# Kernel tuning notes

Measured on AMD Instinct MI355X. Metric: run time of the kernel, lower is better.

## Reference

```python
import jax, jax.numpy as jnp
import numpy as np

D = 1024
H = 16
DH = D // H
SCALE = 1.0 / float(np.sqrt(DH))
EPS = 1e-5


def layer_norm(x, g, b):
    mu = jnp.mean(x, axis=-1, keepdims=True)
    var = jnp.mean((x - mu) ** 2, axis=-1, keepdims=True)
    return (x - mu) * jax.lax.rsqrt(var + EPS) * g + b


def setup_inputs() -> dict:
    key = jax.random.key(0)
    ks = jax.random.split(key, 12)
    B, N = 2, 2048
    x = jax.random.normal(ks[0], (B, N, D), dtype=jnp.float32)
    # sparse 0/1 adjacency (tree-like density) plus self loops
    adj = (jax.random.uniform(ks[1], (B, N, N)) < 0.002).astype(jnp.float32)
    adj = jnp.maximum(adj, jnp.eye(N, dtype=jnp.float32)[None])
    attn_mask = jnp.zeros((B, N, N), dtype=jnp.float32)
    s = 0.02
    params = {
        "qkv_w": jax.random.normal(ks[2], (D, 3 * D)) * s,
        "qkv_b": jnp.zeros((3 * D,), jnp.float32),
        "out_w": jax.random.normal(ks[3], (D, D)) * s,
        "out_b": jnp.zeros((D,), jnp.float32),
        "ln1_g": jnp.ones((D,), jnp.float32),
        "ln1_b": jnp.zeros((D,), jnp.float32),
        "ln2_g": jnp.ones((D,), jnp.float32),
        "ln2_b": jnp.zeros((D,), jnp.float32),
        "ff1_w": jax.random.normal(ks[4], (D, 4 * D)) * s,
        "ff1_b": jnp.zeros((4 * D,), jnp.float32),
        "ff2_w": jax.random.normal(ks[5], (4 * D, D)) * s,
        "ff2_b": jnp.zeros((D,), jnp.float32),
        "struct_bias": jnp.zeros((1,), jnp.float32) + 0.1,
    }
    return {"x": x, "adjacency": adj, "attn_mask": attn_mask, **params}


def reference(x, adjacency, attn_mask, qkv_w, qkv_b, out_w, out_b,
              ln1_g, ln1_b, ln2_g, ln2_b, ff1_w, ff1_b, ff2_w, ff2_b,
              struct_bias):
    b, n, d = x.shape
    residual = x
    h = layer_norm(x, ln1_g, ln1_b)
    qkv = (h @ qkv_w + qkv_b).reshape(b, n, 3, H, DH)
    q = jnp.transpose(qkv[:, :, 0], (0, 2, 1, 3))  # [B,H,N,Dh]
    k = jnp.transpose(qkv[:, :, 1], (0, 2, 1, 3))
    v = jnp.transpose(qkv[:, :, 2], (0, 2, 1, 3))
    scores = jnp.einsum("bhqd,bhkd->bhqk", q, k) * SCALE
    scores = scores + struct_bias[0] * adjacency[:, None] + attn_mask[:, None]
    attn = jax.nn.softmax(scores, axis=-1)  # dropout is identity at eval
    out = jnp.einsum("bhqk,bhkd->bhqd", attn, v)
    out = jnp.transpose(out, (0, 2, 1, 3)).reshape(b, n, d)
    out = out @ out_w + out_b
    x1 = residual + out
    h2 = layer_norm(x1, ln2_g, ln2_b)
    ff = jax.nn.gelu(h2 @ ff1_w + ff1_b, approximate=False) @ ff2_w + ff2_b
    return x1 + ff
```

## Files before the change

kernel.cpp:

```cpp
#include <hip/hip_runtime.h>
#include <math.h>

#define Dm 1024
#define Hh 16
#define DHh 64
#define Bb 2
#define Nn 2048
#define Rr 4096
#define SCALE_ 0.125f
#define EPS_ 1e-5f
#define SMAX_ 4.0f
#define LOG2E_ 1.4426950408889634f

typedef unsigned short u16;
typedef __attribute__((ext_vector_type(8))) short short8;
typedef __attribute__((ext_vector_type(4))) float f32x4;

__device__ __forceinline__ u16 f2bf(float f) {
  union { float f; unsigned u; } v; v.f = f;
  unsigned r = v.u + 0x7fffu + ((v.u >> 16) & 1u);
  return (u16)(r >> 16);
}
__device__ __forceinline__ float bf2f(u16 h) {
  union { unsigned u; float f; } v; v.u = ((unsigned)h) << 16;
  return v.f;
}
__device__ __forceinline__ unsigned pk2(float a, float b) {
  union { float f; unsigned u; } x, y; x.f = a; y.f = b;
  return (x.u >> 16) | (y.u & 0xffff0000u);
}

__device__ __forceinline__ void g2l16(const u16* g, const u16* l) {
  __builtin_amdgcn_global_load_lds(
      (const __attribute__((address_space(1))) void*)g,
      (__attribute__((address_space(3))) void*)l, 16, 0, 0);
}

__global__ void transpose_all(const float* __restrict__ qkv_w, const float* __restrict__ out_w,
                              const float* __restrict__ ff1_w, const float* __restrict__ ff2_w,
                              u16* __restrict__ qkvT, u16* __restrict__ outT,
                              u16* __restrict__ ff1T, u16* __restrict__ ff2T) {
  __shared__ float tile[32][33];
  int flat = blockIdx.x;
  const float* W; u16* WT; int K, N, local;
  if (flat < 3072)        { W = qkv_w; WT = qkvT; K = 1024; N = 3072; local = flat; }
  else if (flat < 4096)   { W = out_w; WT = outT; K = 1024; N = 1024; local = flat - 3072; }
  else if (flat < 8192)   { W = ff1_w; WT = ff1T; K = 1024; N = 4096; local = flat - 4096; }
  else                    { W = ff2_w; WT = ff2T; K = 4096; N = 1024; local = flat - 8192; }
  int nx = N / 32;
  int n0 = (local % nx) * 32, k0 = (local / nx) * 32;
  int tx = threadIdx.x, ty = threadIdx.y;
#pragma unroll
  for (int i = 0; i < 4; i++)
    tile[ty + 8 * i][tx] = W[(size_t)(k0 + ty + 8 * i) * N + n0 + tx];
  __syncthreads();
#pragma unroll
  for (int i = 0; i < 4; i++)
    WT[(size_t)(n0 + ty + 8 * i) * K + k0 + tx] = f2bf(tile[tx][ty + 8 * i]);
}

__global__ void bias_precompute(const float* __restrict__ adj, const float* __restrict__ mask,
                                const float* __restrict__ sbp, u16* __restrict__ bias16) {
  const float sb = sbp[0];
  const float C3 = -SMAX_ * LOG2E_;
  size_t i = ((size_t)blockIdx.x * 256 + threadIdx.x) * 8;
  float4 a0 = *(const float4*)(adj + i);
  float4 a1 = *(const float4*)(adj + i + 4);
  float4 m0 = *(const float4*)(mask + i);
  float4 m1 = *(const float4*)(mask + i + 4);
  ushort4 o0, o1;
  o0.x = f2bf(fmaf(fmaf(sb, a0.x, m0.x), LOG2E_, C3));
  o0.y = f2bf(fmaf(fmaf(sb, a0.y, m0.y), LOG2E_, C3));
  o0.z = f2bf(fmaf(fmaf(sb, a0.z, m0.z), LOG2E_, C3));
  o0.w = f2bf(fmaf(fmaf(sb, a0.w, m0.w), LOG2E_, C3));
  o1.x = f2bf(fmaf(fmaf(sb, a1.x, m1.x), LOG2E_, C3));
  o1.y = f2bf(fmaf(fmaf(sb, a1.y, m1.y), LOG2E_, C3));
  o1.z = f2bf(fmaf(fmaf(sb, a1.z, m1.z), LOG2E_, C3));
  o1.w = f2bf(fmaf(fmaf(sb, a1.w, m1.w), LOG2E_, C3));
  *(ushort4*)(bias16 + i) = o0;
  *(ushort4*)(bias16 + i + 4) = o1;
}

template <int BI>
__global__ void ln_kernel(const void* __restrict__ xin, const float* __restrict__ g,
                          const float* __restrict__ be, u16* __restrict__ out) {
  int row = blockIdx.x;
  int t = threadIdx.x;
  float4 v;
  if (BI) {
    ushort4 uv = ((const ushort4*)((const u16*)xin + (size_t)row * Dm))[t];
    v.x = bf2f(uv.x); v.y = bf2f(uv.y); v.z = bf2f(uv.z); v.w = bf2f(uv.w);
  } else {
    v = ((const float4*)((const float*)xin + (size_t)row * Dm))[t];
  }
  float s = v.x + v.y + v.z + v.w;
  float s2 = v.x * v.x + v.y * v.y + v.z * v.z + v.w * v.w;
#pragma unroll
  for (int o = 32; o > 0; o >>= 1) { s += __shfl_down(s, o); s2 += __shfl_down(s2, o); }
  __shared__ float sm[8];
  int w = t >> 6;
  if ((t & 63) == 0) { sm[w] = s; sm[4 + w] = s2; }
  __syncthreads();
  if (t == 0) {
    float a = sm[0] + sm[1] + sm[2] + sm[3];
    float a2 = sm[4] + sm[5] + sm[6] + sm[7];
    float mu = a * (1.f / Dm);
    sm[0] = mu;
    sm[1] = rsqrtf(a2 * (1.f / Dm) - mu * mu + EPS_);
  }
  __syncthreads();
  float mu = sm[0], rstd = sm[1];
  float4 gv = ((const float4*)g)[t];
  float4 bv = ((const float4*)be)[t];
  ushort4 o4;
  o4.x = f2bf((v.x - mu) * rstd * gv.x + bv.x);
  o4.y = f2bf((v.y - mu) * rstd * gv.y + bv.y);
  o4.z = f2bf((v.z - mu) * rstd * gv.z + bv.z);
  o4.w = f2bf((v.w - mu) * rstd * gv.w + bv.w);
  ((ushort4*)(out + (size_t)row * Dm))[t] = o4;
}

template <int MODE, int MI, int NI>
__global__ __launch_bounds__(256) void gemm_bt(
    const u16* __restrict__ A, const u16* __restrict__ BT,
    const float* __restrict__ bias, const void* __restrict__ res,
    void* __restrict__ Cout, u16* __restrict__ qb,
    u16* __restrict__ kb, u16* __restrict__ vb, int Ndim, int Kdim) {
  constexpr int TM = MI * 32, TN = NI * 32;
  constexpr int NS = (TM + TN) / 16;
  __shared__ u16 As[2][TM * 32];
  __shared__ u16 Bs[2][TN * 32];
  const int t = threadIdx.x;
  const int wave = t >> 6, lane = t & 63;
  const int wm = wave >> 1, wn = wave & 1;
  const int lr = lane & 15, lq = lane >> 4;
  const int flat = blockIdx.x + gridDim.x * blockIdx.y;
  constexpr int nMb = 4096 / TM;
  constexpr int mpx = nMb / 8;
  const int xcd = flat & 7;
  const int p = flat >> 3;
  const int m0 = (xcd * mpx + (p % mpx)) * TM;
  const int n0 = (p / mpx) * TN;

  auto stage = [&](int kt, int bsel) {
#pragma unroll
    for (int s = wave; s < NS; s += 4) {
      if (s < TM / 16)
        g2l16(A + (size_t)(m0 + s * 16 + (lane >> 2)) * Kdim + kt + (lane & 3) * 8,
              &As[bsel][(s * 16) * 32]);
      else
        g2l16(BT + (size_t)(n0 + (s - TM / 16) * 16 + (lane >> 2)) * Kdim + kt + (lane & 3) * 8,
              &Bs[bsel][((s - TM / 16) * 16) * 32]);
    }
  };

  f32x4 acc[MI][NI];
#pragma unroll
  for (int i = 0; i < MI; i++)
#pragma unroll
    for (int j = 0; j < NI; j++) acc[i][j] = (f32x4){0.f, 0.f, 0.f, 0.f};

  stage(0, 0);
  int cur = 0;
  for (int kt = 0; kt < Kdim; kt += 32) {
    __syncthreads();
    if (kt + 32 < Kdim) stage(kt + 32, cur ^ 1);
    short8 af[MI], bf[NI];
#pragma unroll
    for (int i = 0; i < MI; i++)
      af[i] = *(const short8*)&As[cur][(wm * (MI * 16) + i * 16 + lr) * 32 + lq * 8];
#pragma unroll
    for (int j = 0; j < NI; j++)
      bf[j] = *(const short8*)&Bs[cur][(wn * (NI * 16) + j * 16 + lr) * 32 + lq * 8];
#pragma unroll
    for (int i = 0; i < MI; i++)
#pragma unroll
      for (int j = 0; j < NI; j++)
        acc[i][j] = __builtin_amdgcn_mfma_f32_16x16x32_bf16(af[i], bf[j], acc[i][j], 0, 0, 0);
    cur ^= 1;
  }

#pragma unroll
  for (int i = 0; i < MI; i++) {
#pragma unroll
    for (int j = 0; j < NI; j++) {
#pragma unroll
      for (int r = 0; r < 4; r++) {
        int row = m0 + wm * (MI * 16) + i * 16 + lq * 4 + r;
        int col = n0 + wn * (NI * 16) + j * 16 + lr;
        float val = acc[i][j][r] + bias[col];
        if (MODE == 0) {
          int s = col >> 10, rem = col & 1023;
          int hh = rem >> 6, dh = rem & 63;
          int bi = row >> 11, ni = row & 2047;
          if (s == 2) {
            vb[(((size_t)bi * Hh + hh) * DHh + dh) * Nn + ni] = f2bf(val);
          } else {
            u16* dst = (s == 0) ? qb : kb;
            dst[(((size_t)bi * Hh + hh) * Nn + ni) * DHh + dh] = f2bf(val);
          }
        } else if (MODE == 1) {
          size_t o = (size_t)row * Ndim + col;
          ((u16*)Cout)[o] = f2bf(val + ((const float*)res)[o]);
        } else if (MODE == 3) {
          size_t o = (size_t)row * Ndim + col;
          ((float*)Cout)[o] = val + bf2f(((const u16*)res)[o]);
        } else {
          float u = val;
          float y2 = 1.5957691216f * fmaf(0.044715f * u, u * u, u);
          float gv = u / (1.f + __expf(-y2));
          size_t o = (size_t)row * Ndim + col;
          ((u16*)Cout)[o] = f2bf(gv);
        }
      }
    }
  }
}

__global__ __launch_bounds__(256) void attn_kernel(
    const u16* __restrict__ q, const u16* __restrict__ k, const u16* __restrict__ vT,
    const u16* __restrict__ bias16, u16* __restrict__ pO0, u16* __restrict__ pO1,
    float* __restrict__ pl) {
  const int qt = blockIdx.x, hb = blockIdx.y, kp = blockIdx.z;
  const int hh = hb & 15, b = hb >> 4;
  const int t = threadIdx.x, wave = t >> 6, lane = t & 63;
  const int lr = lane & 15, lq = lane >> 4;
  const size_t head_off = (((size_t)b * Hh + hh) * Nn) * DHh;
  const u16* Q = q + head_off;
  const u16* K = k + head_off;
  const u16* Vt = vT + head_off;
  const int q0 = qt * 128;
  const int kbase = kp * (Nn / 2);
  u16* pO = kp ? pO1 : pO0;

  __shared__ u16 Ks[64 * 72];
  __shared__ u16 VsT[64 * 72];
  __shared__ u16 Ps[4][32 * 72];

  short8 qf[2][2];
#pragma unroll
  for (int qs = 0; qs < 2; qs++) {
    const u16* Qr = Q + (size_t)(q0 + wave * 32 + qs * 16 + lr) * DHh;
    qf[qs][0] = *(const short8*)(Qr + lq * 8);
    qf[qs][1] = *(const short8*)(Qr + 32 + lq * 8);
  }
  f32x4 o_acc[2][4];
  float l_acc[2];
#pragma unroll
  for (int qs = 0; qs < 2; qs++) {
#pragma unroll
    for (int j = 0; j < 4; j++) o_acc[qs][j] = (f32x4){0.f, 0.f, 0.f, 0.f};
    l_acc[qs] = 0.f;
  }

  const int srow = t >> 2;
  const int sc0 = (t & 3) * 16;
  const int ssw = ((srow >> 2) & 3) << 4;
  const int wc0 = sc0 ^ ssw, wc1 = (sc0 + 8) ^ ssw;
  const u16* Kst = K + (size_t)srow * DHh + sc0;
  const u16* Vst = Vt + (size_t)srow * Nn + sc0;
  const int rsw = ((lr >> 2) & 3) << 4;

  const u16* bp = bias16 + ((size_t)b * Nn + q0 + wave * 32 + lr) * Nn;

  f32x4 kr0 = *(const f32x4*)(Kst + (size_t)kbase * DHh);
  f32x4 kr1 = *(const f32x4*)(Kst + (size_t)kbase * DHh + 8);
  f32x4 vr0 = *(const f32x4*)(Vst + kbase);
  f32x4 vr1 = *(const f32x4*)(Vst + kbase + 8);
  ushort4 bw[2][4];
#pragma unroll
  for (int qs = 0; qs < 2; qs++)
#pragma unroll
    for (int ns = 0; ns < 4; ns++)
      bw[qs][ns] = *(const ushort4*)(bp + (size_t)qs * 16 * Nn + kbase + ns * 16 + lq * 4);

  const float C1 = SCALE_ * LOG2E_;
  const int kend = kbase + Nn / 2;

  for (int kt = kbase; kt < kend; kt += 64) {
    __syncthreads();
    *(f32x4*)&Ks[srow * 72 + wc0] = kr0;
    *(f32x4*)&Ks[srow * 72 + wc1] = kr1;
    *(f32x4*)&VsT[srow * 72 + wc0] = vr0;
    *(f32x4*)&VsT[srow * 72 + wc1] = vr1;
    __syncthreads();
    if (kt + 64 < kend) {
      kr0 = *(const f32x4*)(Kst + (size_t)(kt + 64) * DHh);
      kr1 = *(const f32x4*)(Kst + (size_t)(kt + 64) * DHh + 8);
      vr0 = *(const f32x4*)(Vst + kt + 64);
      vr1 = *(const f32x4*)(Vst + kt + 64 + 8);
    }
    short8 kf[4][2];
#pragma unroll
    for (int ns = 0; ns < 4; ns++) {
      int row = ns * 16 + lr;
      kf[ns][0] = *(const short8*)&Ks[row * 72 + ((lq * 8) ^ rsw)];
      kf[ns][1] = *(const short8*)&Ks[row * 72 + ((32 + lq * 8) ^ rsw)];
    }
    f32x4 s0[4], s1[4];
#pragma unroll
    for (int ns = 0; ns < 4; ns++) {
      f32x4 z = (f32x4){0.f, 0.f, 0.f, 0.f};
      s0[ns] = __builtin_amdgcn_mfma_f32_16x16x32_bf16(kf[ns][0], qf[0][0], z, 0, 0, 0);
      s0[ns] = __builtin_amdgcn_mfma_f32_16x16x32_bf16(kf[ns][1], qf[0][1], s0[ns], 0, 0, 0);
      s1[ns] = __builtin_amdgcn_mfma_f32_16x16x32_bf16(kf[ns][0], qf[1][0], z, 0, 0, 0);
      s1[ns] = __builtin_amdgcn_mfma_f32_16x16x32_bf16(kf[ns][1], qf[1][1], s1[ns], 0, 0, 0);
    }
    float p0[4][4], p1[4][4];
#pragma unroll
    for (int ns = 0; ns < 4; ns++) {
      p0[ns][0] = exp2f(fmaf(s0[ns][0], C1, bf2f(bw[0][ns].x)));
      p0[ns][1] = exp2f(fmaf(s0[ns][1], C1, bf2f(bw[0][ns].y)));
      p0[ns][2] = exp2f(fmaf(s0[ns][2], C1, bf2f(bw[0][ns].z)));
      p0[ns][3] = exp2f(fmaf(s0[ns][3], C1, bf2f(bw[0][ns].w)));
      p1[ns][0] = exp2f(fmaf(s1[ns][0], C1, bf2f(bw[1][ns].x)));
      p1[ns][1] = exp2f(fmaf(s1[ns][1], C1, bf2f(bw[1][ns].y)));
      p1[ns][2] = exp2f(fmaf(s1[ns][2], C1, bf2f(bw[1][ns].z)));
      p1[ns][3] = exp2f(fmaf(s1[ns][3], C1, bf2f(bw[1][ns].w)));
      l_acc[0] += (p0[ns][0] + p0[ns][1]) + (p0[ns][2] + p0[ns][3]);
      l_acc[1] += (p1[ns][0] + p1[ns][1]) + (p1[ns][2] + p1[ns][3]);
    }
    if (kt + 64 < kend) {
#pragma unroll
      for (int qs = 0; qs < 2; qs++)
#pragma unroll
        for (int ns = 0; ns < 4; ns++)
          bw[qs][ns] = *(const ushort4*)(bp + (size_t)qs * 16 * Nn + kt + 64 + ns * 16 + lq * 4);
    }
#pragma unroll
    for (int ns = 0; ns < 4; ns++) {
      int sc = ((ns ^ ((lr >> 2) & 3)) << 4) + lq * 4;
      uint2 w0, w1;
      w0.x = pk2(p0[ns][0], p0[ns][1]); w0.y = pk2(p0[ns][2], p0[ns][3]);
      w1.x = pk2(p1[ns][0], p1[ns][1]); w1.y = pk2(p1[ns][2], p1[ns][3]);
      *(uint2*)&Ps[wave][lr * 72 + sc] = w0;
      *(uint2*)&Ps[wave][(16 + lr) * 72 + sc] = w1;
    }
    short8 pf[2][2];
#pragma unroll
    for (int qs = 0; qs < 2; qs++) {
      pf[qs][0] = *(const short8*)&Ps[wave][(qs * 16 + lr) * 72 + ((lq * 8) ^ rsw)];
      pf[qs][1] = *(const short8*)&Ps[wave][(qs * 16 + lr) * 72 + ((32 + lq * 8) ^ rsw)];
    }
#pragma unroll
    for (int j = 0; j < 4; j++) {
      int row = j * 16 + lr;
      short8 vf0 = *(const short8*)&VsT[row * 72 + ((lq * 8) ^ rsw)];
      short8 vf1 = *(const short8*)&VsT[row * 72 + ((32 + lq * 8) ^ rsw)];
      o_acc[0][j] = __builtin_amdgcn_mfma_f32_16x16x32_bf16(pf[0][0], vf0, o_acc[0][j], 0, 0, 0);
      o_acc[0][j] = __builtin_amdgcn_mfma_f32_16x16x32_bf16(pf[0][1], vf1, o_acc[0][j], 0, 0, 0);
      o_acc[1][j] = __builtin_amdgcn_mfma_f32_16x16x32_bf16(pf[1][0], vf0, o_acc[1][j], 0, 0, 0);
      o_acc[1][j] = __builtin_amdgcn_mfma_f32_16x16x32_bf16(pf[1][1], vf1, o_acc[1][j], 0, 0, 0);
    }
  }
#pragma unroll
  for (int qs = 0; qs < 2; qs++) {
    float l = l_acc[qs];
    l += __shfl_xor(l, 16);
    l += __shfl_xor(l, 32);
    if (lane < 16)
      pl[((size_t)(kp * Bb + b) * Hh + hh) * Nn + q0 + wave * 32 + qs * 16 + lr] = l;
#pragma unroll
    for (int r = 0; r < 4; r++) {
      int qrow = q0 + wave * 32 + qs * 16 + lq * 4 + r;
#pragma unroll
      for (int j = 0; j < 4; j++) {
        pO[((size_t)(b * Nn + qrow)) * Dm + hh * DHh + j * 16 + lr] =
            f2bf(o_acc[qs][j][r]);
      }
    }
  }
}

__global__ void attn_combine(const u16* __restrict__ pO0, const u16* __restrict__ pO1,
                             const float* __restrict__ pl, u16* __restrict__ ao) {
  int row = blockIdx.x;
  int t = threadIdx.x;
  int col = t * 4;
  int b = row >> 11, n = row & 2047, hh = col >> 6;
  size_t li = ((size_t)b * Hh + hh) * Nn + n;
  float inv = 1.f / (pl[li] + pl[(size_t)Bb * Hh * Nn + li]);
  ushort4 a0 = *(const ushort4*)(pO0 + (size_t)row * Dm + col);
  ushort4 a1 = *(const ushort4*)(pO1 + (size_t)row * Dm + col);
  ushort4 o;
  o.x = f2bf((bf2f(a0.x) + bf2f(a1.x)) * inv);
  o.y = f2bf((bf2f(a0.y) + bf2f(a1.y)) * inv);
  o.z = f2bf((bf2f(a0.z) + bf2f(a1.z)) * inv);
  o.w = f2bf((bf2f(a0.w) + bf2f(a1.w)) * inv);
  *(ushort4*)(ao + (size_t)row * Dm + col) = o;
}

extern "C" void kernel_launch(void* const* d_in, const int* in_sizes, int n_in,
                              void* d_out, int out_size, void* d_ws, size_t ws_size,
                              hipStream_t stream) {
  const float* x     = (const float*)d_in[0];
  const float* adj   = (const float*)d_in[1];
  const float* amask = (const float*)d_in[2];
  const float* qkv_w = (const float*)d_in[3];
  const float* qkv_b = (const float*)d_in[4];
  const float* out_w = (const float*)d_in[5];
  const float* out_b = (const float*)d_in[6];
  const float* ln1_g = (const float*)d_in[7];
  const float* ln1_b = (const float*)d_in[8];
  const float* ln2_g = (const float*)d_in[9];
  const float* ln2_b = (const float*)d_in[10];
  const float* ff1_w = (const float*)d_in[11];
  const float* ff1_b = (const float*)d_in[12];
  const float* ff2_w = (const float*)d_in[13];
  const float* ff2_b = (const float*)d_in[14];
  const float* sbias = (const float*)d_in[15];

  char* w = (char*)d_ws;
  const size_t MB = 1024 * 1024;
  u16* h      = (u16*)(w);
  u16* qb     = (u16*)(w + 8 * MB);
  u16* kb     = (u16*)(w + 16 * MB);
  u16* vb     = (u16*)(w + 24 * MB);
  u16* ao     = (u16*)(w + 32 * MB);
  float* pl   = (float*)(w + 40 * MB);
  u16* x1     = (u16*)(w + 40 * MB);
  u16* pO0    = (u16*)(w + 48 * MB);
  u16* pO1    = h;
  u16* qkvT   = (u16*)(w + 56 * MB);
  u16* outT   = (u16*)(w + 62 * MB);
  u16* ff1T   = (u16*)(w + 64 * MB);
  u16* ff2T   = (u16*)(w + 72 * MB);
  u16* bias16 = (u16*)(w + 80 * MB);
  u16* ffo    = qb;

  transpose_all<<<dim3(12288), dim3(32, 8), 0, stream>>>(
      qkv_w, out_w, ff1_w, ff2_w, qkvT, outT, ff1T, ff2T);

  bias_precompute<<<dim3((Bb * Nn * Nn) / (8 * 256)), dim3(256), 0, stream>>>(adj, amask, sbias, bias16);

  ln_kernel<0><<<dim3(Rr), dim3(256), 0, stream>>>(x, ln1_g, ln1_b, h);

  gemm_bt<0, 4, 4><<<dim3(3072 / 128, 4096 / 128), dim3(256), 0, stream>>>(
      h, qkvT, qkv_b, nullptr, nullptr, qb, kb, vb, 3072, 1024);

  attn_kernel<<<dim3(16, 32, 2), dim3(256), 0, stream>>>(qb, kb, vb, bias16, pO0, pO1, pl);

  attn_combine<<<dim3(Rr), dim3(256), 0, stream>>>(pO0, pO1, pl, ao);

  gemm_bt<1, 4, 2><<<dim3(1024 / 64, 4096 / 128), dim3(256), 0, stream>>>(
      ao, outT, out_b, x, (void*)x1, nullptr, nullptr, nullptr, 1024, 1024);

  ln_kernel<1><<<dim3(Rr), dim3(256), 0, stream>>>(x1, ln2_g, ln2_b, h);

  gemm_bt<2, 4, 4><<<dim3(4096 / 128, 4096 / 128), dim3(256), 0, stream>>>(
      h, ff1T, ff1_b, nullptr, (void*)ffo, nullptr, nullptr, nullptr, 4096, 1024);

  gemm_bt<3, 4, 2><<<dim3(1024 / 64, 4096 / 128), dim3(256), 0, stream>>>(
      ffo, ff2T, ff2_b, x1, d_out, nullptr, nullptr, nullptr, 1024, 4096);
}
```

Measured before the change: 464.6 us.

## Load K and V fragments directly from global memory instead of staging in LDS

The attention kernel no longer stages K and V tiles in shared memory with block-wide barriers and register prefetch. Each wave now reads its MFMA operands straight from global memory (relying on L1/L2 caching, since the four waves share the same K/V). Bias loads move into the loop without a prefetch, and the loop is unrolled by two. This removes the two __syncthreads per tile and the LDS traffic, at the cost of redundant global loads across waves and exposed load latency with no software prefetch.

```diff
diff --git a/kernel.cpp b/kernel.cpp
--- a/kernel.cpp
+++ b/kernel.cpp
@@ -233,8 +233,6 @@
   const int kbase = kp * (Nn / 2);
   u16* pO = kp ? pO1 : pO0;
 
-  __shared__ u16 Ks[64 * 72];
-  __shared__ u16 VsT[64 * 72];
   __shared__ u16 Ps[4][32 * 72];
 
   short8 qf[2][2];
@@ -253,86 +251,44 @@
     l_acc[qs] = 0.f;
   }
 
-  const int srow = t >> 2;
-  const int sc0 = (t & 3) * 16;
-  const int ssw = ((srow >> 2) & 3) << 4;
-  const int wc0 = sc0 ^ ssw, wc1 = (sc0 + 8) ^ ssw;
-  const u16* Kst = K + (size_t)srow * DHh + sc0;
-  const u16* Vst = Vt + (size_t)srow * Nn + sc0;
   const int rsw = ((lr >> 2) & 3) << 4;
-
   const u16* bp = bias16 + ((size_t)b * Nn + q0 + wave * 32 + lr) * Nn;
-
-  f32x4 kr0 = *(const f32x4*)(Kst + (size_t)kbase * DHh);
-  f32x4 kr1 = *(const f32x4*)(Kst + (size_t)kbase * DHh + 8);
-  f32x4 vr0 = *(const f32x4*)(Vst + kbase);
-  f32x4 vr1 = *(const f32x4*)(Vst + kbase + 8);
-  ushort4 bw[2][4];
-#pragma unroll
-  for (int qs = 0; qs < 2; qs++)
-#pragma unroll
-    for (int ns = 0; ns < 4; ns++)
-      bw[qs][ns] = *(const ushort4*)(bp + (size_t)qs * 16 * Nn + kbase + ns * 16 + lq * 4);
-
   const float C1 = SCALE_ * LOG2E_;
   const int kend = kbase + Nn / 2;
 
+#pragma unroll 2
   for (int kt = kbase; kt < kend; kt += 64) {
-    __syncthreads();
-    *(f32x4*)&Ks[srow * 72 + wc0] = kr0;
-    *(f32x4*)&Ks[srow * 72 + wc1] = kr1;
-    *(f32x4*)&VsT[srow * 72 + wc0] = vr0;
-    *(f32x4*)&VsT[srow * 72 + wc1] = vr1;
-    __syncthreads();
-    if (kt + 64 < kend) {
-      kr0 = *(const f32x4*)(Kst + (size_t)(kt + 64) * DHh);
-      kr1 = *(const f32x4*)(Kst + (size_t)(kt + 64) * DHh + 8);
-      vr0 = *(const f32x4*)(Vst + kt + 64);
-      vr1 = *(const f32x4*)(Vst + kt + 64 + 8);
-    }
-    short8 kf[4][2];
+    ushort4 bw[2][4];
+#pragma unroll
+    for (int qs = 0; qs < 2; qs++)
+#pragma unroll
+      for (int ns = 0; ns < 4; ns++)
+        bw[qs][ns] = *(const ushort4*)(bp + (size_t)qs * 16 * Nn + kt + ns * 16 + lq * 4);
+
 #pragma unroll
     for (int ns = 0; ns < 4; ns++) {
-      int row = ns * 16 + lr;
-      kf[ns][0] = *(const short8*)&Ks[row * 72 + ((lq * 8) ^ rsw)];
-      kf[ns][1] = *(const short8*)&Ks[row * 72 + ((32 + lq * 8) ^ rsw)];
-    }
-    f32x4 s0[4], s1[4];
-#pragma unroll
-    for (int ns = 0; ns < 4; ns++) {
+      const u16* Kr = K + (size_t)(kt + ns * 16 + lr) * DHh + lq * 8;
+      short8 k0 = *(const short8*)Kr;
+      short8 k1 = *(const short8*)(Kr + 32);
       f32x4 z = (f32x4){0.f, 0.f, 0.f, 0.f};
-      s0[ns] = __builtin_amdgcn_mfma_f32_16x16x32_bf16(kf[ns][0], qf[0][0], z, 0, 0, 0);
-      s0[ns] = __builtin_amdgcn_mfma_f32_16x16x32_bf16(kf[ns][1], qf[0][1], s0[ns], 0, 0, 0);
-      s1[ns] = __builtin_amdgcn_mfma_f32_16x16x32_bf16(kf[ns][0], qf[1][0], z, 0, 0, 0);
-      s1[ns] = __builtin_amdgcn_mfma_f32_16x16x32_bf16(kf[ns][1], qf[1][1], s1[ns], 0, 0, 0);
-    }
-    float p0[4][4], p1[4][4];
-#pragma unroll
-    for (int ns = 0; ns < 4; ns++) {
-      p0[ns][0] = exp2f(fmaf(s0[ns][0], C1, bf2f(bw[0][ns].x)));
-      p0[ns][1] = exp2f(fmaf(s0[ns][1], C1, bf2f(bw[0][ns].y)));
-      p0[ns][2] = exp2f(fmaf(s0[ns][2], C1, bf2f(bw[0][ns].z)));
-      p0[ns][3] = exp2f(fmaf(s0[ns][3], C1, bf2f(bw[0][ns].w)));
-      p1[ns][0] = exp2f(fmaf(s1[ns][0], C1, bf2f(bw[1][ns].x)));
-      p1[ns][1] = exp2f(fmaf(s1[ns][1], C1, bf2f(bw[1][ns].y)));
-      p1[ns][2] = exp2f(fmaf(s1[ns][2], C1, bf2f(bw[1][ns].z)));
-      p1[ns][3] = exp2f(fmaf(s1[ns][3], C1, bf2f(bw[1][ns].w)));
-      l_acc[0] += (p0[ns][0] + p0[ns][1]) + (p0[ns][2] + p0[ns][3]);
-      l_acc[1] += (p1[ns][0] + p1[ns][1]) + (p1[ns][2] + p1[ns][3]);
-    }
-    if (kt + 64 < kend) {
-#pragma unroll
-      for (int qs = 0; qs < 2; qs++)
-#pragma unroll
-        for (int ns = 0; ns < 4; ns++)
-          bw[qs][ns] = *(const ushort4*)(bp + (size_t)qs * 16 * Nn + kt + 64 + ns * 16 + lq * 4);
-    }
-#pragma unroll
-    for (int ns = 0; ns < 4; ns++) {
+      f32x4 s0 = __builtin_amdgcn_mfma_f32_16x16x32_bf16(k0, qf[0][0], z, 0, 0, 0);
+      s0 = __builtin_amdgcn_mfma_f32_16x16x32_bf16(k1, qf[0][1], s0, 0, 0, 0);
+      f32x4 s1 = __builtin_amdgcn_mfma_f32_16x16x32_bf16(k0, qf[1][0], z, 0, 0, 0);
+      s1 = __builtin_amdgcn_mfma_f32_16x16x32_bf16(k1, qf[1][1], s1, 0, 0, 0);
+      float p00 = exp2f(fmaf(s0[0], C1, bf2f(bw[0][ns].x)));
+      float p01 = exp2f(fmaf(s0[1], C1, bf2f(bw[0][ns].y)));
+      float p02 = exp2f(fmaf(s0[2], C1, bf2f(bw[0][ns].z)));
+      float p03 = exp2f(fmaf(s0[3], C1, bf2f(bw[0][ns].w)));
+      float p10 = exp2f(fmaf(s1[0], C1, bf2f(bw[1][ns].x)));
+      float p11 = exp2f(fmaf(s1[1], C1, bf2f(bw[1][ns].y)));
+      float p12 = exp2f(fmaf(s1[2], C1, bf2f(bw[1][ns].z)));
+      float p13 = exp2f(fmaf(s1[3], C1, bf2f(bw[1][ns].w)));
+      l_acc[0] += (p00 + p01) + (p02 + p03);
+      l_acc[1] += (p10 + p11) + (p12 + p13);
       int sc = ((ns ^ ((lr >> 2) & 3)) << 4) + lq * 4;
       uint2 w0, w1;
-      w0.x = pk2(p0[ns][0], p0[ns][1]); w0.y = pk2(p0[ns][2], p0[ns][3]);
-      w1.x = pk2(p1[ns][0], p1[ns][1]); w1.y = pk2(p1[ns][2], p1[ns][3]);
+      w0.x = pk2(p00, p01); w0.y = pk2(p02, p03);
+      w1.x = pk2(p10, p11); w1.y = pk2(p12, p13);
       *(uint2*)&Ps[wave][lr * 72 + sc] = w0;
       *(uint2*)&Ps[wave][(16 + lr) * 72 + sc] = w1;
     }
@@ -344,9 +300,9 @@
     }
 #pragma unroll
     for (int j = 0; j < 4; j++) {
-      int row = j * 16 + lr;
-      short8 vf0 = *(const short8*)&VsT[row * 72 + ((lq * 8) ^ rsw)];
-      short8 vf1 = *(const short8*)&VsT[row * 72 + ((32 + lq * 8) ^ rsw)];
+      const u16* Vr = Vt + (size_t)(j * 16 + lr) * Nn + kt + lq * 8;
+      short8 vf0 = *(const short8*)Vr;
+      short8 vf1 = *(const short8*)(Vr + 32);
       o_acc[0][j] = __builtin_amdgcn_mfma_f32_16x16x32_bf16(pf[0][0], vf0, o_acc[0][j], 0, 0, 0);
       o_acc[0][j] = __builtin_amdgcn_mfma_f32_16x16x32_bf16(pf[0][1], vf1, o_acc[0][j], 0, 0, 0);
       o_acc[1][j] = __builtin_amdgcn_mfma_f32_16x16x32_bf16(pf[1][0], vf0, o_acc[1][j], 0, 0, 0);
```

After: 548.7 us. 18.1% more time.

## Double-buffer attention K/V tiles with direct global-to-LDS loads and MFMA priority

Applied to the files above, without the earlier changes.

The attention kernel now keeps K and V^T tiles in two LDS buffers and fills the next buffer with asynchronous global-to-LDS copies (g2l16) while the current tile is processed. This removes the register round trip and one barrier per iteration. The padded stride-72 layout becomes an unpadded stride-64 layout with an XOR swizzle to avoid bank conflicts. s_setprio is raised around the MFMA blocks to favour matrix issue. The risks are correctness of the async-copy waits, since there is one barrier per loop and g2l16 completion must be tracked, and the extra LDS reducing occupancy.

```diff
diff --git a/kernel.cpp b/kernel.cpp
--- a/kernel.cpp
+++ b/kernel.cpp
@@ -233,8 +233,8 @@
   const int kbase = kp * (Nn / 2);
   u16* pO = kp ? pO1 : pO0;
 
-  __shared__ u16 Ks[64 * 72];
-  __shared__ u16 VsT[64 * 72];
+  __shared__ u16 Ks[2][64 * 64];
+  __shared__ u16 VsT[2][64 * 64];
   __shared__ u16 Ps[4][32 * 72];
 
   short8 qf[2][2];
@@ -253,20 +253,27 @@
     l_acc[qs] = 0.f;
   }
 
-  const int srow = t >> 2;
-  const int sc0 = (t & 3) * 16;
-  const int ssw = ((srow >> 2) & 3) << 4;
-  const int wc0 = sc0 ^ ssw, wc1 = (sc0 + 8) ^ ssw;
-  const u16* Kst = K + (size_t)srow * DHh + sc0;
-  const u16* Vst = Vt + (size_t)srow * Nn + sc0;
+  const int lsub = lane >> 3;
+  const int xch = ((lane & 7) ^ lsub) * 8;
+
+  auto stage = [&](int kt, int bsel) {
+#pragma unroll
+    for (int i = 0; i < 4; i++) {
+      const int s = wave + i * 4;
+      if (s < 8)
+        g2l16(K + (size_t)(kt + s * 8 + lsub) * DHh + xch, &Ks[bsel][s * 512]);
+      else
+        g2l16(Vt + (size_t)((s - 8) * 8 + lsub) * Nn + kt + xch,
+              &VsT[bsel][(s - 8) * 512]);
+    }
+  };
+
   const int rsw = ((lr >> 2) & 3) << 4;
-
+  const int kx = lr & 7;
   const u16* bp = bias16 + ((size_t)b * Nn + q0 + wave * 32 + lr) * Nn;
-
-  f32x4 kr0 = *(const f32x4*)(Kst + (size_t)kbase * DHh);
-  f32x4 kr1 = *(const f32x4*)(Kst + (size_t)kbase * DHh + 8);
-  f32x4 vr0 = *(const f32x4*)(Vst + kbase);
-  f32x4 vr1 = *(const f32x4*)(Vst + kbase + 8);
+  const float C1 = SCALE_ * LOG2E_;
+  const int kend = kbase + Nn / 2;
+
   ushort4 bw[2][4];
 #pragma unroll
   for (int qs = 0; qs < 2; qs++)
@@ -274,30 +281,23 @@
     for (int ns = 0; ns < 4; ns++)
       bw[qs][ns] = *(const ushort4*)(bp + (size_t)qs * 16 * Nn + kbase + ns * 16 + lq * 4);
 
-  const float C1 = SCALE_ * LOG2E_;
-  const int kend = kbase + Nn / 2;
-
+  stage(kbase, 0);
+  int cur = 0;
   for (int kt = kbase; kt < kend; kt += 64) {
     __syncthreads();
-    *(f32x4*)&Ks[srow * 72 + wc0] = kr0;
-    *(f32x4*)&Ks[srow * 72 + wc1] = kr1;
-    *(f32x4*)&VsT[srow * 72 + wc0] = vr0;
-    *(f32x4*)&VsT[srow * 72 + wc1] = vr1;
-    __syncthreads();
-    if (kt + 64 < kend) {
-      kr0 = *(const f32x4*)(Kst + (size_t)(kt + 64) * DHh);
-      kr1 = *(const f32x4*)(Kst + (size_t)(kt + 64) * DHh + 8);
-      vr0 = *(const f32x4*)(Vst + kt + 64);
-      vr1 = *(const f32x4*)(Vst + kt + 64 + 8);
-    }
+    if (kt + 64 < kend) stage(kt + 64, cur ^ 1);
+    const u16* Kc = Ks[cur];
+    const u16* Vc = VsT[cur];
+
     short8 kf[4][2];
 #pragma unroll
     for (int ns = 0; ns < 4; ns++) {
-      int row = ns * 16 + lr;
-      kf[ns][0] = *(const short8*)&Ks[row * 72 + ((lq * 8) ^ rsw)];
-      kf[ns][1] = *(const short8*)&Ks[row * 72 + ((32 + lq * 8) ^ rsw)];
+      int R = ns * 16 + lr;
+      kf[ns][0] = *(const short8*)&Kc[R * 64 + ((lq ^ kx) * 8)];
+      kf[ns][1] = *(const short8*)&Kc[R * 64 + (((4 + lq) ^ kx) * 8)];
     }
     f32x4 s0[4], s1[4];
+    __builtin_amdgcn_s_setprio(1);
 #pragma unroll
     for (int ns = 0; ns < 4; ns++) {
       f32x4 z = (f32x4){0.f, 0.f, 0.f, 0.f};
@@ -306,6 +306,8 @@
       s1[ns] = __builtin_amdgcn_mfma_f32_16x16x32_bf16(kf[ns][0], qf[1][0], z, 0, 0, 0);
       s1[ns] = __builtin_amdgcn_mfma_f32_16x16x32_bf16(kf[ns][1], qf[1][1], s1[ns], 0, 0, 0);
     }
+    __builtin_amdgcn_s_setprio(0);
+
     float p0[4][4], p1[4][4];
 #pragma unroll
     for (int ns = 0; ns < 4; ns++) {
@@ -344,14 +346,17 @@
     }
 #pragma unroll
     for (int j = 0; j < 4; j++) {
-      int row = j * 16 + lr;
-      short8 vf0 = *(const short8*)&VsT[row * 72 + ((lq * 8) ^ rsw)];
-      short8 vf1 = *(const short8*)&VsT[row * 72 + ((32 + lq * 8) ^ rsw)];
+      int R = j * 16 + lr;
+      short8 vf0 = *(const short8*)&Vc[R * 64 + ((lq ^ kx) * 8)];
+      short8 vf1 = *(const short8*)&Vc[R * 64 + (((4 + lq) ^ kx) * 8)];
+      __builtin_amdgcn_s_setprio(1);
       o_acc[0][j] = __builtin_amdgcn_mfma_f32_16x16x32_bf16(pf[0][0], vf0, o_acc[0][j], 0, 0, 0);
       o_acc[0][j] = __builtin_amdgcn_mfma_f32_16x16x32_bf16(pf[0][1], vf1, o_acc[0][j], 0, 0, 0);
       o_acc[1][j] = __builtin_amdgcn_mfma_f32_16x16x32_bf16(pf[1][0], vf0, o_acc[1][j], 0, 0, 0);
       o_acc[1][j] = __builtin_amdgcn_mfma_f32_16x16x32_bf16(pf[1][1], vf1, o_acc[1][j], 0, 0, 0);
-    }
+      __builtin_amdgcn_s_setprio(0);
+    }
+    cur ^= 1;
   }
 #pragma unroll
   for (int qs = 0; qs < 2; qs++) {
```

Result: faster. 452.0 us (-2.7%).
